# Optimization experiments

Hardware: AMD Instinct MI355X
Metric: run time of the kernel (lower is better)

## Reference

```python
import jax, jax.numpy as jnp
import numpy as np

B, F, Hh, Ww, C = 1, 8, 12, 18, 1920
HEADS, HD, RANK, TXT = 30, 64, 128, 224
VID = F * Hh * Ww  # 1728
DN = ('NCH', 'OIH', 'NCH')


def setup_inputs() -> dict:
    key = jax.random.key(0)
    ks = jax.random.split(key, 14)
    s = 0.02
    return {
        'hidden_states': jax.random.normal(ks[0], (B, VID, C), jnp.float32),
        'encoder_hidden_states': jax.random.normal(ks[1], (B, TXT, C), jnp.float32),
        'cos': jax.random.uniform(ks[2], (VID, HD), jnp.float32),
        'sin': jax.random.uniform(ks[3], (VID, HD), jnp.float32),
        'conv1_w': jax.random.normal(ks[4], (RANK, C, 3), jnp.float32) * s,
        'conv2_w': jax.random.normal(ks[5], (C, RANK, 3), jnp.float32) * s,
        'Wq': jax.random.normal(ks[6], (C, C), jnp.float32) * s,
        'bq': jnp.zeros((C,), jnp.float32),
        'Wk': jax.random.normal(ks[7], (C, C), jnp.float32) * s,
        'bk': jnp.zeros((C,), jnp.float32),
        'Wv': jax.random.normal(ks[8], (C, C), jnp.float32) * s,
        'bv': jnp.zeros((C,), jnp.float32),
        'Wo': jax.random.normal(ks[9], (C, C), jnp.float32) * s,
        'bo': jnp.zeros((C,), jnp.float32),
    }


def _rope(x, cos, sin):
    # x: [B, H, S_vid, D]; cos/sin: [S_vid, D]; interleaved rotate-half
    xr = x.reshape(*x.shape[:-1], -1, 2)
    x_rot = jnp.stack([-xr[..., 1], xr[..., 0]], axis=-1).reshape(x.shape)
    return x * cos + x_rot * sin


def reference(hidden_states, encoder_hidden_states, cos, sin, conv1_w, conv2_w,
              Wq, bq, Wk, bk, Wv, bv, Wo, bo):
    # temporal conv1d skip branch over frame axis per spatial location
    x = hidden_states.reshape(B, F, Hh, Ww, C).transpose(0, 2, 3, 4, 1)
    x = x.reshape(B * Hh * Ww, C, F)
    h = jax.lax.conv_general_dilated(x, conv1_w, (1,), [(1, 1)], dimension_numbers=DN)
    h = jax.nn.gelu(h, approximate=False)
    h = jax.lax.conv_general_dilated(h, conv2_w, (1,), [(1, 1)], dimension_numbers=DN)
    skip = h.reshape(B, Hh, Ww, C, F).transpose(0, 4, 1, 2, 3).reshape(B, VID, C)

    hs = jnp.concatenate([encoder_hidden_states, hidden_states + skip], axis=1)  # [B,S,C]

    q = (hs @ Wq.T + bq).reshape(B, -1, HEADS, HD).transpose(0, 2, 1, 3)
    k = (hs @ Wk.T + bk).reshape(B, -1, HEADS, HD).transpose(0, 2, 1, 3)
    v = (hs @ Wv.T + bv).reshape(B, -1, HEADS, HD).transpose(0, 2, 1, 3)

    # RoPE applied only to the video (image) tokens of q and k
    q = jnp.concatenate([q[:, :, :TXT], _rope(q[:, :, TXT:], cos, sin)], axis=2)
    k = jnp.concatenate([k[:, :, :TXT], _rope(k[:, :, TXT:], cos, sin)], axis=2)

    scores = jnp.einsum('bhqd,bhkd->bhqk', q, k) * (HD ** -0.5)
    attn = jax.nn.softmax(scores, axis=-1)
    o = jnp.einsum('bhqk,bhkd->bhqd', attn, v)
    o = o.transpose(0, 2, 1, 3).reshape(B, -1, HEADS * HD)
    o = o @ Wo.T + bo  # to_out[0]; to_out[1] is dropout (identity at eval)

    return (o[:, TXT:], o[:, :TXT])  # (hidden_states, encoder_hidden_states)
```

## Files before the change

kernel.cpp:

```cpp
#include <hip/hip_runtime.h>
#include <math.h>

typedef unsigned short u16;
typedef short short8 __attribute__((ext_vector_type(8)));
typedef short shortv4 __attribute__((ext_vector_type(4)));
typedef float f32x4 __attribute__((ext_vector_type(4)));

#define TXT 224
#define VID 1728
#define S_ALL 1952
#define C_DIM 1920
#define HD 64
#define RANK 128
#define SHD 124928

#define OFF_HS   ((size_t)0)
#define OFF_XPAD ((size_t)3932160)
#define OFF_O    OFF_XPAD
#define OFF_HG   ((size_t)8355840)
#define OFF_W1T  ((size_t)8650752)
#define OFF_W2T  ((size_t)9388032)
#define OFF_WQ   ((size_t)10125312)
#define OFF_WK   ((size_t)13811712)
#define OFF_WV   ((size_t)17498112)
#define OFF_WO   ((size_t)21184512)
#define OFF_Q    ((size_t)24870912)
#define OFF_K    ((size_t)28618752)
#define OFF_V    ((size_t)32366592)

__device__ __forceinline__ float b2f(u16 u) {
  union { unsigned int i; float f; } x; x.i = ((unsigned int)u) << 16; return x.f;
}
__device__ __forceinline__ u16 f2b(float f) {
  union { float f; unsigned int i; } x; x.f = f;
  unsigned int i = x.i;
  return (u16)((i + 0x7FFFu + ((i >> 16) & 1u)) >> 16);
}
__device__ __forceinline__ void gload16(const u16* g, short* l) {
  __builtin_amdgcn_global_load_lds((const __attribute__((address_space(1))) unsigned int*)g,
                                   (__attribute__((address_space(3))) unsigned int*)l, 16, 0, 0);
}

__global__ void __launch_bounds__(256) prep_kernel(const float* __restrict__ hidden,
                                                   const float* __restrict__ enc,
                                                   const float* __restrict__ w1,
                                                   const float* __restrict__ w2,
                                                   const float* __restrict__ Wq,
                                                   const float* __restrict__ Wk,
                                                   const float* __restrict__ Wv,
                                                   const float* __restrict__ Wo,
                                                   u16* __restrict__ ws) {
  size_t i = (size_t)blockIdx.x * 256 + threadIdx.x;
  if (i < 1105920) {
    const size_t e = i * 4;
    const int row = (int)(e / 1920), col = (int)(e % 1920);
    shortv4 o4 = {0, 0, 0, 0};
    if (row >= 216 && row < 1944) {
      const float4 f = *(const float4*)(hidden + (size_t)(row - 216) * 1920 + col);
      o4 = (shortv4){(short)f2b(f.x), (short)f2b(f.y), (short)f2b(f.z), (short)f2b(f.w)};
    }
    *(shortv4*)(ws + OFF_XPAD + e) = o4;
    return;
  }
  i -= 1105920;
  if (i < 184320) {
    const size_t e = i * 4;
    const int r = (int)(e / 5760), j = (int)(e % 5760), t = j / 1920, c = j % 1920;
    const float* s = w1 + (size_t)r * 5760 + (size_t)c * 3 + t;
    shortv4 o4 = {(short)f2b(s[0]), (short)f2b(s[3]), (short)f2b(s[6]), (short)f2b(s[9])};
    *(shortv4*)(ws + OFF_W1T + e) = o4;
    return;
  }
  i -= 184320;
  if (i < 184320) {
    const size_t e = i * 4;
    const int c = (int)(e / 384), j = (int)(e % 384), t = j / 128, r = j % 128;
    const float* s = w2 + (size_t)c * 384 + (size_t)r * 3 + t;
    shortv4 o4 = {(short)f2b(s[0]), (short)f2b(s[3]), (short)f2b(s[6]), (short)f2b(s[9])};
    *(shortv4*)(ws + OFF_W2T + e) = o4;
    return;
  }
  i -= 184320;
  if (i < 107520) {
    const size_t e = i * 4;
    const float4 f = *(const float4*)(enc + e);
    *(shortv4*)(ws + OFF_HS + e) =
        (shortv4){(short)f2b(f.x), (short)f2b(f.y), (short)f2b(f.z), (short)f2b(f.w)};
    return;
  }
  i -= 107520;
  if (i < 3686400) {
    const int j = (int)(i / 921600);
    const size_t e = (i - (size_t)j * 921600) * 4;
    const float* src = (j == 0) ? Wq : ((j == 1) ? Wk : ((j == 2) ? Wv : Wo));
    const float4 f = *(const float4*)(src + e);
    *(shortv4*)(ws + OFF_WQ + (size_t)j * 3686400 + e) =
        (shortv4){(short)f2b(f.x), (short)f2b(f.y), (short)f2b(f.z), (short)f2b(f.w)};
    return;
  }
  i -= 3686400;
  const short8 z8 = {0, 0, 0, 0, 0, 0, 0, 0};
  size_t e;
  if (i < 23040) e = OFF_HS + 3747840 + i * 8;
  else if (i < 26496) e = OFF_HG + (i - 23040) * 8;
  else if (i < 32256) e = OFF_HG + 248832 + (i - 26496) * 8;
  else e = OFF_O + 3747840 + (i - 32256) * 8;
  *(short8*)(ws + e) = z8;
}

struct GArgs {
  const u16 *A, *B0, *B1, *B2;
  const float *bias0, *bias1, *bias2;
  const float *cosp, *sinp, *hidden;
  u16 *out0, *out1, *out2;
  float* outf;
  int lda, ldb, ksteps, spt, tap_rows, nMt, nNt, Mvalid;
};

template <int BM, int BN, int EPI>
__global__ void __launch_bounds__(256) gemm_bt(GArgs a) {
  constexpr int WM = BM / 2, WN = BN / 2, FM = WM / 16, FN = WN / 16;
  __shared__ __align__(16) short lA[2][BM * 32];
  __shared__ __align__(16) short lB[2][BN * 32];
  const int tid = threadIdx.x;
  const int lane = tid & 63;
  const int wv = tid >> 6, wr = wv >> 1, wc = wv & 1;
  const int lr = lane & 15, lg = lane >> 4;
  const int nwg = (int)gridDim.x;
  const int qq = nwg >> 3, rr = nwg & 7;
  const int xx = (int)blockIdx.x & 7, ssb = (int)blockIdx.x >> 3;
  const int bswz = (xx < rr ? xx * (qq + 1) : rr * (qq + 1) + (xx - rr) * qq) + ssb;
  const int mtile = bswz % a.nMt;
  const int ntile_raw = bswz / a.nMt;
  const int ntile = ntile_raw % a.nNt;
  const int slice = ntile_raw / a.nNt;
  const int kstart = slice * a.ksteps;
  const int sec = (ntile * BN) / C_DIM;
  const u16* Bw = (sec == 0) ? a.B0 : ((sec == 1) ? a.B1 : a.B2);
  const int nb = ntile * BN - sec * C_DIM;
  const int m0 = mtile * BM;

  f32x4 acc[FM][FN];
#pragma unroll
  for (int i = 0; i < FM; ++i)
#pragma unroll
    for (int j = 0; j < FN; ++j) acc[i][j] = (f32x4){0.f, 0.f, 0.f, 0.f};

  auto stageStep = [&](int buf, int gs) {
    const int tap = gs / a.spt;
    const int kcol = (gs - tap * a.spt) * 32;
    const int arow0 = m0 + tap * a.tap_rows;
#pragma unroll
    for (int i = 0; i < BM / 64; ++i) {
      const int o = (i * 256 + tid) * 16;
      const int row = o >> 6;
      const int ke = (o & 63) >> 1;
      gload16(a.A + (size_t)(arow0 + row) * a.lda + (kcol + ke), &lA[buf][o >> 1]);
    }
#pragma unroll
    for (int i = 0; i < BN / 64; ++i) {
      const int o = (i * 256 + tid) * 16;
      const int row = o >> 6;
      const int ke = (o & 63) >> 1;
      gload16(Bw + (size_t)(nb + row) * a.ldb + (gs * 32 + ke), &lB[buf][o >> 1]);
    }
  };

  stageStep(0, kstart);
  __syncthreads();
  int cur = 0;
  for (int s = 0; s < a.ksteps; ++s) {
    if (s + 1 < a.ksteps) stageStep(cur ^ 1, kstart + s + 1);
    short8 af[FM], bfr[FN];
#pragma unroll
    for (int i = 0; i < FM; ++i)
      af[i] = *(const short8*)(&lA[cur][(wr * WM + i * 16 + lr) * 32 + lg * 8]);
#pragma unroll
    for (int j = 0; j < FN; ++j)
      bfr[j] = *(const short8*)(&lB[cur][(wc * WN + j * 16 + lr) * 32 + lg * 8]);
#pragma unroll
    for (int i = 0; i < FM; ++i)
#pragma unroll
      for (int j = 0; j < FN; ++j)
        acc[i][j] = __builtin_amdgcn_mfma_f32_16x16x32_bf16(af[i], bfr[j], acc[i][j], 0, 0, 0);
    __syncthreads();
    cur ^= 1;
  }

#pragma unroll
  for (int i = 0; i < FM; ++i) {
#pragma unroll
    for (int j = 0; j < FN; ++j) {
      const int col = ntile * BN + wc * WN + j * 16 + lr;
#pragma unroll
      for (int r = 0; r < 4; ++r) {
        const int m = m0 + wr * WM + i * 16 + lg * 4 + r;
        float v = acc[i][j][r];
        if (EPI == 4) {
          if (m < a.Mvalid) a.outf[(size_t)slice * 221184 + (size_t)m * RANK + col] = v;
        } else if (EPI == 1) {
          if (m < a.Mvalid) {
            v += a.hidden[(size_t)m * C_DIM + col];
            a.out0[(size_t)m * C_DIM + col] = f2b(v);
          }
        } else if (EPI == 2) {
          const int nn = col - sec * C_DIM;
          const int hh = nn >> 6, d = nn & 63;
          const float* bias = (sec == 0) ? a.bias0 : ((sec == 1) ? a.bias1 : a.bias2);
          v += bias[nn];
          const float vp = __shfl_xor(v, 1);
          if (sec < 2 && m >= TXT) {
            const int vid = ((m < S_ALL) ? m : TXT) - TXT;
            const float c = a.cosp[vid * HD + d];
            const float sn = a.sinp[vid * HD + d];
            v = (d & 1) ? (v * c + vp * sn) : (v * c - vp * sn);
          }
          if (sec == 0) v *= 0.18033688011112042f;
          if (m < a.Mvalid) {
            u16* dst = (sec == 0) ? a.out0 : ((sec == 1) ? a.out1 : a.out2);
            dst[(size_t)hh * SHD + (size_t)m * HD + d] = f2b(v);
          }
        } else {
          v += a.bias0[col];
          if (m < a.Mvalid) {
            const int dr = (m >= TXT) ? (m - TXT) : (VID + m);
            a.outf[(size_t)dr * C_DIM + col] = v;
          }
        }
      }
    }
  }
}

__global__ void __launch_bounds__(256) c1reduce_kernel(const float* __restrict__ part,
                                                       u16* __restrict__ hg) {
  const int i = blockIdx.x * 256 + threadIdx.x;
  float s = 0.f;
#pragma unroll
  for (int j = 0; j < 6; ++j) s += part[(size_t)j * 221184 + i];
  const float g = 0.5f * s * (1.0f + erff(s * 0.70710678f));
  hg[i] = f2b(g);
}

__global__ void __launch_bounds__(256) vtrans_kernel(const u16* __restrict__ vin,
                                                     u16* __restrict__ vout) {
  __shared__ u16 t[64][72];
  const int b = blockIdx.x, hh = b / 31, mt = b % 31;
  const int m0 = mt * 64;
  const int rows = (m0 + 64 <= S_ALL) ? 64 : (S_ALL - m0);
  const int tid = threadIdx.x;
  const u16* src = vin + (size_t)hh * SHD + (size_t)m0 * HD;
#pragma unroll
  for (int p = 0; p < 2; ++p) {
    const int r = p * 32 + (tid >> 3), c = (tid & 7) * 8;
    short8 v8 = {0, 0, 0, 0, 0, 0, 0, 0};
    if (r < rows) v8 = *(const short8*)(src + (size_t)r * HD + c);
    *(short8*)&t[r][c] = v8;
  }
  __syncthreads();
  const int d = tid & 63, ms = tid >> 6;
  if (ms * 16 < rows) {
    short8 a0, a1;
#pragma unroll
    for (int x = 0; x < 8; ++x) { a0[x] = (short)t[ms * 16 + x][d]; a1[x] = (short)t[ms * 16 + 8 + x][d]; }
    u16* dst = vout + (size_t)hh * SHD + (size_t)d * S_ALL + m0 + ms * 16;
    *(short8*)dst = a0;
    *(short8*)(dst + 8) = a1;
  }
}

__global__ void __launch_bounds__(256) attn_kernel(const u16* __restrict__ q,
                                                   const u16* __restrict__ k,
                                                   const u16* __restrict__ vT,
                                                   u16* __restrict__ o) {
  __shared__ __align__(16) short lK[2][4096];
  __shared__ __align__(16) short lV[2][4096];
  __shared__ __align__(16) short lp[4][1024];
  const int xcd = blockIdx.x & 7, idx = blockIdx.x >> 3;
  const int bid = (xcd < 2) ? (xcd * 117 + idx) : (234 + (xcd - 2) * 116 + idx);
  const int hh = bid / 31, qt = bid - hh * 31;
  const int tid = threadIdx.x, wv = tid >> 6, lane = tid & 63;
  const int lr = lane & 15, lg = lane >> 4;
  const int qbase = qt * 64 + wv * 16;
  const bool active = qbase < S_ALL;
  const u16* qh = q + (size_t)hh * SHD;
  const u16* kh = k + (size_t)hh * SHD;
  const u16* vh = vT + (size_t)hh * SHD;

  int krow[2], kcol[2], kdst[2];
#pragma unroll
  for (int j = 0; j < 2; ++j) {
    const int p0 = (j * 256 + tid) * 8;
    const int row = p0 >> 6, cs = p0 & 63;
    kdst[j] = p0;
    krow[j] = row;
    kcol[j] = cs ^ ((row & 7) * 8);
  }

  short8 aq0 = {}, aq1 = {};
  if (active) {
    aq0 = *(const short8*)(qh + (size_t)(qbase + lr) * HD + lg * 8);
    aq1 = *(const short8*)(qh + (size_t)(qbase + lr) * HD + 32 + lg * 8);
  }
  f32x4 oa[4];
#pragma unroll
  for (int gd = 0; gd < 4; ++gd) oa[gd] = (f32x4){0.f, 0.f, 0.f, 0.f};
  float lw = 0.f;
  const f32x4 z4 = (f32x4){0.f, 0.f, 0.f, 0.f};
  const int pmask = (lr & 7) * 8;
  short* lpw = &lp[wv][0];

#pragma unroll
  for (int j = 0; j < 2; ++j) gload16(kh + (size_t)krow[j] * HD + kcol[j], &lK[0][kdst[j]]);
#pragma unroll
  for (int j = 0; j < 2; ++j) gload16(vh + (size_t)krow[j] * S_ALL + kcol[j], &lV[0][kdst[j]]);
  __syncthreads();

  int cur = 0;
  for (int t = 0; t < 30; ++t) {
    const int kb = t * 64;
    if (t < 29) {
#pragma unroll
      for (int j = 0; j < 2; ++j)
        gload16(kh + (size_t)(kb + 64 + krow[j]) * HD + kcol[j], &lK[cur ^ 1][kdst[j]]);
#pragma unroll
      for (int j = 0; j < 2; ++j)
        gload16(vh + (size_t)krow[j] * S_ALL + (kb + 64 + kcol[j]), &lV[cur ^ 1][kdst[j]]);
    }
    if (active) {
      const short* Kt = &lK[cur][0];
      const short* Vt = &lV[cur][0];
      f32x4 st[4];
      __builtin_amdgcn_s_setprio(1);
#pragma unroll
      for (int k16 = 0; k16 < 4; ++k16) {
        const int row = k16 * 16 + lr;
        const int m8 = (row & 7) * 8;
        short8 kf0 = *(const short8*)(Kt + row * 64 + ((lg * 8) ^ m8));
        short8 kf1 = *(const short8*)(Kt + row * 64 + ((32 + lg * 8) ^ m8));
        st[k16] = __builtin_amdgcn_mfma_f32_16x16x32_bf16(kf0, aq0, z4, 0, 0, 0);
        st[k16] = __builtin_amdgcn_mfma_f32_16x16x32_bf16(kf1, aq1, st[k16], 0, 0, 0);
      }
      __builtin_amdgcn_s_setprio(0);
      float rs = 0.f;
#pragma unroll
      for (int k16 = 0; k16 < 4; ++k16) {
        float p0 = __builtin_exp2f(st[k16][0]);
        float p1 = __builtin_exp2f(st[k16][1]);
        float p2 = __builtin_exp2f(st[k16][2]);
        float p3 = __builtin_exp2f(st[k16][3]);
        rs += (p0 + p1) + (p2 + p3);
        uint2 pk;
        asm("v_cvt_pk_bf16_f32 %0, %1, %2" : "=v"(pk.x) : "v"(p0), "v"(p1));
        asm("v_cvt_pk_bf16_f32 %0, %1, %2" : "=v"(pk.y) : "v"(p2), "v"(p3));
        *(uint2*)(lpw + lr * 64 + ((k16 * 16 + lg * 4) ^ pmask)) = pk;
      }
      rs += __shfl_xor(rs, 16);
      rs += __shfl_xor(rs, 32);
      lw += rs;
      asm volatile("s_waitcnt lgkmcnt(0)" ::: "memory");
      short8 pa0 = *(const short8*)(lpw + lr * 64 + ((lg * 8) ^ pmask));
      short8 pa1 = *(const short8*)(lpw + lr * 64 + ((32 + lg * 8) ^ pmask));
      __builtin_amdgcn_s_setprio(1);
#pragma unroll
      for (int gd = 0; gd < 4; ++gd) {
        const int row = gd * 16 + lr;
        const int m8 = (row & 7) * 8;
        short8 vf0 = *(const short8*)(Vt + row * 64 + ((lg * 8) ^ m8));
        short8 vf1 = *(const short8*)(Vt + row * 64 + ((32 + lg * 8) ^ m8));
        f32x4 tacc = __builtin_amdgcn_mfma_f32_16x16x32_bf16(pa0, vf0, oa[gd], 0, 0, 0);
        oa[gd] = __builtin_amdgcn_mfma_f32_16x16x32_bf16(pa1, vf1, tacc, 0, 0, 0);
      }
      __builtin_amdgcn_s_setprio(0);
    }
    __syncthreads();
    cur ^= 1;
  }

  if (active) {
    const u16* kp = kh + (size_t)1920 * HD;
    short8 kf00 = *(const short8*)(kp + (size_t)lr * HD + lg * 8);
    short8 kf01 = *(const short8*)(kp + (size_t)lr * HD + 32 + lg * 8);
    short8 kf10 = *(const short8*)(kp + (size_t)(16 + lr) * HD + lg * 8);
    short8 kf11 = *(const short8*)(kp + (size_t)(16 + lr) * HD + 32 + lg * 8);
    f32x4 st0 = __builtin_amdgcn_mfma_f32_16x16x32_bf16(kf00, aq0, z4, 0, 0, 0);
    st0 = __builtin_amdgcn_mfma_f32_16x16x32_bf16(kf01, aq1, st0, 0, 0, 0);
    f32x4 st1 = __builtin_amdgcn_mfma_f32_16x16x32_bf16(kf10, aq0, z4, 0, 0, 0);
    st1 = __builtin_amdgcn_mfma_f32_16x16x32_bf16(kf11, aq1, st1, 0, 0, 0);
    float rs = 0.f;
    float pp[8];
#pragma unroll
    for (int r = 0; r < 4; ++r) { pp[r] = __builtin_exp2f(st0[r]); rs += pp[r]; }
#pragma unroll
    for (int r = 0; r < 4; ++r) { pp[4 + r] = __builtin_exp2f(st1[r]); rs += pp[4 + r]; }
    {
      uint2 pk;
      asm("v_cvt_pk_bf16_f32 %0, %1, %2" : "=v"(pk.x) : "v"(pp[0]), "v"(pp[1]));
      asm("v_cvt_pk_bf16_f32 %0, %1, %2" : "=v"(pk.y) : "v"(pp[2]), "v"(pp[3]));
      *(uint2*)(lpw + lr * 64 + ((lg * 4) ^ pmask)) = pk;
      asm("v_cvt_pk_bf16_f32 %0, %1, %2" : "=v"(pk.x) : "v"(pp[4]), "v"(pp[5]));
      asm("v_cvt_pk_bf16_f32 %0, %1, %2" : "=v"(pk.y) : "v"(pp[6]), "v"(pp[7]));
      *(uint2*)(lpw + lr * 64 + ((16 + lg * 4) ^ pmask)) = pk;
    }
    rs += __shfl_xor(rs, 16);
    rs += __shfl_xor(rs, 32);
    lw += rs;
    asm volatile("s_waitcnt lgkmcnt(0)" ::: "memory");
    short8 pa0 = *(const short8*)(lpw + lr * 64 + ((lg * 8) ^ pmask));
#pragma unroll
    for (int gd = 0; gd < 4; ++gd) {
      short8 vf = *(const short8*)(vh + (size_t)(gd * 16 + lr) * S_ALL + 1920 + lg * 8);
      oa[gd] = __builtin_amdgcn_mfma_f32_16x16x32_bf16(pa0, vf, oa[gd], 0, 0, 0);
    }
    float lwp[4];
#pragma unroll
    for (int r = 0; r < 4; ++r) lwp[r] = 1.0f / __shfl(lw, lg * 4 + r);
#pragma unroll
    for (int gd = 0; gd < 4; ++gd) {
      const int col = hh * HD + gd * 16 + lr;
#pragma unroll
      for (int r = 0; r < 4; ++r) {
        const int m = qbase + lg * 4 + r;
        o[(size_t)m * C_DIM + col] = f2b(oa[gd][r] * lwp[r]);
      }
    }
  }
}

extern "C" void kernel_launch(void* const* d_in, const int* in_sizes, int n_in,
                              void* d_out, int out_size, void* d_ws, size_t ws_size,
                              hipStream_t stream) {
  const float* hidden = (const float*)d_in[0];
  const float* enc = (const float*)d_in[1];
  const float* cosp = (const float*)d_in[2];
  const float* sinp = (const float*)d_in[3];
  const float* w1 = (const float*)d_in[4];
  const float* w2 = (const float*)d_in[5];
  const float* bq = (const float*)d_in[7];
  const float* bk = (const float*)d_in[9];
  const float* bv = (const float*)d_in[11];
  const float* bo = (const float*)d_in[13];
  u16* ws = (u16*)d_ws;
  float* out = (float*)d_out;

  prep_kernel<<<20796, 256, 0, stream>>>(hidden, enc, w1, w2, (const float*)d_in[6],
                                         (const float*)d_in[8], (const float*)d_in[10],
                                         (const float*)d_in[12], ws);

  GArgs c1{};
  c1.A = ws + OFF_XPAD; c1.B0 = c1.B1 = c1.B2 = ws + OFF_W1T;
  c1.lda = C_DIM; c1.ldb = 5760; c1.ksteps = 30; c1.spt = 60; c1.tap_rows = 216;
  c1.nMt = 27; c1.nNt = 2; c1.Mvalid = VID;
  c1.outf = (float*)(ws + OFF_Q);
  gemm_bt<64, 64, 4><<<324, 256, 0, stream>>>(c1);

  c1reduce_kernel<<<864, 256, 0, stream>>>((const float*)(ws + OFF_Q),
                                           ws + OFF_HG + (size_t)216 * RANK);

  GArgs c2{};
  c2.A = ws + OFF_HG; c2.B0 = c2.B1 = c2.B2 = ws + OFF_W2T;
  c2.lda = RANK; c2.ldb = 384; c2.ksteps = 12; c2.spt = 4; c2.tap_rows = 216;
  c2.nMt = 14; c2.nNt = 15; c2.Mvalid = VID; c2.hidden = hidden;
  c2.out0 = ws + OFF_HS + (size_t)TXT * C_DIM;
  gemm_bt<128, 128, 1><<<210, 256, 0, stream>>>(c2);

  GArgs c3{};
  c3.A = ws + OFF_HS; c3.B0 = ws + OFF_WQ; c3.B1 = ws + OFF_WK; c3.B2 = ws + OFF_WV;
  c3.bias0 = bq; c3.bias1 = bk; c3.bias2 = bv; c3.cosp = cosp; c3.sinp = sinp;
  c3.lda = C_DIM; c3.ldb = C_DIM; c3.ksteps = 60; c3.spt = 60; c3.tap_rows = 0;
  c3.nMt = 16; c3.nNt = 45; c3.Mvalid = S_ALL;
  c3.out0 = ws + OFF_Q; c3.out1 = ws + OFF_K; c3.out2 = ws + OFF_O;
  gemm_bt<128, 128, 2><<<720, 256, 0, stream>>>(c3);

  vtrans_kernel<<<930, 256, 0, stream>>>(ws + OFF_O, ws + OFF_V);

  attn_kernel<<<930, 256, 0, stream>>>(ws + OFF_Q, ws + OFF_K, ws + OFF_V, ws + OFF_O);

  GArgs c4{};
  c4.A = ws + OFF_O; c4.B0 = c4.B1 = c4.B2 = ws + OFF_WO; c4.bias0 = bo;
  c4.lda = C_DIM; c4.ldb = C_DIM; c4.ksteps = 60; c4.spt = 60; c4.tap_rows = 0;
  c4.nMt = 32; c4.nNt = 15; c4.Mvalid = S_ALL;
  c4.outf = out;
  gemm_bt<64, 128, 3><<<480, 256, 0, stream>>>(c4);
}
```

Measured before the change: 254.5 us.

## Double K-step per LDS stage with XOR swizzle; split-K output projection via atomics

The GEMM template gains a KU parameter that stages 64 K-elements per LDS buffer, halving the barriers and stage steps per tile, and applies an XOR swizzle to the LDS layout to avoid bank conflicts. The QKV GEMM switches to KU=2. The output projection moves to 128x128 tiles with a 2-way split-K, and its partials are accumulated into the zeroed output with float atomicAdd, adding only the bias in slice 0. This adds a memset, atomic traffic and doubled LDS use, which may lower occupancy, and it makes the fp32 summation order nondeterministic.

```diff
diff --git a/kernel.cpp b/kernel.cpp
--- a/kernel.cpp
+++ b/kernel.cpp
@@ -117,11 +117,12 @@
   int lda, ldb, ksteps, spt, tap_rows, nMt, nNt, Mvalid;
 };
 
-template <int BM, int BN, int EPI>
+template <int BM, int BN, int EPI, int KU = 1>
 __global__ void __launch_bounds__(256) gemm_bt(GArgs a) {
   constexpr int WM = BM / 2, WN = BN / 2, FM = WM / 16, FN = WN / 16;
-  __shared__ __align__(16) short lA[2][BM * 32];
-  __shared__ __align__(16) short lB[2][BN * 32];
+  constexpr int KW = 32 * KU;
+  __shared__ __align__(16) short lA[2][BM * KW];
+  __shared__ __align__(16) short lB[2][BN * KW];
   const int tid = threadIdx.x;
   const int lane = tid & 63;
   const int wv = tid >> 6, wr = wv >> 1, wc = wv & 1;
@@ -151,38 +152,51 @@
     const int kcol = (gs - tap * a.spt) * 32;
     const int arow0 = m0 + tap * a.tap_rows;
 #pragma unroll
-    for (int i = 0; i < BM / 64; ++i) {
-      const int o = (i * 256 + tid) * 16;
-      const int row = o >> 6;
-      const int ke = (o & 63) >> 1;
-      gload16(a.A + (size_t)(arow0 + row) * a.lda + (kcol + ke), &lA[buf][o >> 1]);
-    }
-#pragma unroll
-    for (int i = 0; i < BN / 64; ++i) {
-      const int o = (i * 256 + tid) * 16;
-      const int row = o >> 6;
-      const int ke = (o & 63) >> 1;
-      gload16(Bw + (size_t)(nb + row) * a.ldb + (gs * 32 + ke), &lB[buf][o >> 1]);
+    for (int i = 0; i < BM * KU / 64; ++i) {
+      const int c = i * 256 + tid;
+      const int row = c / (4 * KU);
+      int colE = (c % (4 * KU)) * 8;
+      if (KU == 2) colE ^= (row & 7) * 8;
+      gload16(a.A + (size_t)(arow0 + row) * a.lda + (kcol + colE), &lA[buf][c * 8]);
+    }
+#pragma unroll
+    for (int i = 0; i < BN * KU / 64; ++i) {
+      const int c = i * 256 + tid;
+      const int row = c / (4 * KU);
+      int colE = (c % (4 * KU)) * 8;
+      if (KU == 2) colE ^= (row & 7) * 8;
+      gload16(Bw + (size_t)(nb + row) * a.ldb + (gs * 32 + colE), &lB[buf][c * 8]);
     }
   };
 
   stageStep(0, kstart);
   __syncthreads();
   int cur = 0;
-  for (int s = 0; s < a.ksteps; ++s) {
-    if (s + 1 < a.ksteps) stageStep(cur ^ 1, kstart + s + 1);
-    short8 af[FM], bfr[FN];
-#pragma unroll
-    for (int i = 0; i < FM; ++i)
-      af[i] = *(const short8*)(&lA[cur][(wr * WM + i * 16 + lr) * 32 + lg * 8]);
-#pragma unroll
-    for (int j = 0; j < FN; ++j)
-      bfr[j] = *(const short8*)(&lB[cur][(wc * WN + j * 16 + lr) * 32 + lg * 8]);
-#pragma unroll
-    for (int i = 0; i < FM; ++i)
-#pragma unroll
-      for (int j = 0; j < FN; ++j)
-        acc[i][j] = __builtin_amdgcn_mfma_f32_16x16x32_bf16(af[i], bfr[j], acc[i][j], 0, 0, 0);
+  for (int s = 0; s < a.ksteps; s += KU) {
+    if (s + KU < a.ksteps) stageStep(cur ^ 1, kstart + s + KU);
+#pragma unroll
+    for (int u = 0; u < KU; ++u) {
+      short8 af[FM], bfr[FN];
+#pragma unroll
+      for (int i = 0; i < FM; ++i) {
+        const int row = wr * WM + i * 16 + lr;
+        int col = u * 32 + lg * 8;
+        if (KU == 2) col ^= (row & 7) * 8;
+        af[i] = *(const short8*)(&lA[cur][row * KW + col]);
+      }
+#pragma unroll
+      for (int j = 0; j < FN; ++j) {
+        const int row = wc * WN + j * 16 + lr;
+        int col = u * 32 + lg * 8;
+        if (KU == 2) col ^= (row & 7) * 8;
+        bfr[j] = *(const short8*)(&lB[cur][row * KW + col]);
+      }
+#pragma unroll
+      for (int i = 0; i < FM; ++i)
+#pragma unroll
+        for (int j = 0; j < FN; ++j)
+          acc[i][j] = __builtin_amdgcn_mfma_f32_16x16x32_bf16(af[i], bfr[j], acc[i][j], 0, 0, 0);
+    }
     __syncthreads();
     cur ^= 1;
   }
@@ -220,11 +234,11 @@
             u16* dst = (sec == 0) ? a.out0 : ((sec == 1) ? a.out1 : a.out2);
             dst[(size_t)hh * SHD + (size_t)m * HD + d] = f2b(v);
           }
-        } else {
-          v += a.bias0[col];
+        } else if (EPI == 5) {
+          if (slice == 0) v += a.bias0[col];
           if (m < a.Mvalid) {
             const int dr = (m >= TXT) ? (m - TXT) : (VID + m);
-            a.outf[(size_t)dr * C_DIM + col] = v;
+            atomicAdd(&a.outf[(size_t)dr * C_DIM + col], v);
           }
         }
       }
@@ -443,6 +457,8 @@
   u16* ws = (u16*)d_ws;
   float* out = (float*)d_out;
 
+  hipMemsetAsync(d_out, 0, (size_t)out_size * sizeof(float), stream);
+
   prep_kernel<<<20796, 256, 0, stream>>>(hidden, enc, w1, w2, (const float*)d_in[6],
                                          (const float*)d_in[8], (const float*)d_in[10],
                                          (const float*)d_in[12], ws);
@@ -470,7 +486,7 @@
   c3.lda = C_DIM; c3.ldb = C_DIM; c3.ksteps = 60; c3.spt = 60; c3.tap_rows = 0;
   c3.nMt = 16; c3.nNt = 45; c3.Mvalid = S_ALL;
   c3.out0 = ws + OFF_Q; c3.out1 = ws + OFF_K; c3.out2 = ws + OFF_O;
-  gemm_bt<128, 128, 2><<<720, 256, 0, stream>>>(c3);
+  gemm_bt<128, 128, 2, 2><<<720, 256, 0, stream>>>(c3);
 
   vtrans_kernel<<<930, 256, 0, stream>>>(ws + OFF_O, ws + OFF_V);
 
@@ -478,8 +494,8 @@
 
   GArgs c4{};
   c4.A = ws + OFF_O; c4.B0 = c4.B1 = c4.B2 = ws + OFF_WO; c4.bias0 = bo;
-  c4.lda = C_DIM; c4.ldb = C_DIM; c4.ksteps = 60; c4.spt = 60; c4.tap_rows = 0;
-  c4.nMt = 32; c4.nNt = 15; c4.Mvalid = S_ALL;
+  c4.lda = C_DIM; c4.ldb = C_DIM; c4.ksteps = 30; c4.spt = 60; c4.tap_rows = 0;
+  c4.nMt = 16; c4.nNt = 15; c4.Mvalid = S_ALL;
   c4.outf = out;
-  gemm_bt<64, 128, 3><<<480, 256, 0, stream>>>(c4);
-}
+  gemm_bt<128, 128, 5, 2><<<480, 256, 0, stream>>>(c4);
+}
```

Measured after the change: 307.5 us. +20.8%, slower.
